# Kernel tuning notes

Hardware: AMD Instinct MI355X
Metric: run time of the kernel (lower is better)

## Reference

```python
import jax, jax.numpy as jnp
import numpy as np

OWN_DIM = 7
INTR_DIM = 5
N_HEADS = 3
HEAD_DIM = 5
N_INTR = 256
ACT_DIM = 2
HID = 256
B = 16384


def setup_inputs() -> dict:
    key = jax.random.key(0)
    ks = jax.random.split(key, 16)
    def rn(k, shape, scale=0.1):
        return (jax.random.normal(k, shape, dtype=jnp.float32) * scale)
    obs = jax.random.normal(ks[0], (B, OWN_DIM + N_INTR * INTR_DIM), dtype=jnp.float32)
    in_dim = OWN_DIM + N_HEADS * HEAD_DIM  # 22
    return {
        "obs": obs,
        "Wq": rn(ks[1], (N_HEADS, HEAD_DIM, OWN_DIM)),
        "bq": rn(ks[2], (N_HEADS, HEAD_DIM)),
        "Wk": rn(ks[3], (N_HEADS, HEAD_DIM, INTR_DIM)),
        "bk": rn(ks[4], (N_HEADS, HEAD_DIM)),
        "Wv": rn(ks[5], (N_HEADS, HEAD_DIM, INTR_DIM)),
        "bv": rn(ks[6], (N_HEADS, HEAD_DIM)),
        "v_att": rn(ks[7], (N_HEADS, HEAD_DIM), 0.5),
        "temperature": jnp.ones((1,), dtype=jnp.float32) * 3.0,
        "W1": rn(ks[8], (in_dim, HID)),
        "b1": rn(ks[9], (HID,)),
        "W2": rn(ks[10], (HID, HID)),
        "b2": rn(ks[11], (HID,)),
        "Wf": rn(ks[12], (HID, ACT_DIM)),
        "bf": rn(ks[13], (ACT_DIM,)),
        "log_std": jnp.zeros((ACT_DIM,), dtype=jnp.float32),
    }


def reference(obs, Wq, bq, Wk, bk, Wv, bv, v_att, temperature,
              W1, b1, W2, b2, Wf, bf, log_std):
    own = obs[:, :OWN_DIM]                                   # [B,7]
    intr = obs[:, OWN_DIM:OWN_DIM + N_INTR * INTR_DIM].reshape(-1, N_INTR, INTR_DIM)  # [B,N,5]

    # per-head projections, all heads at once
    q = jnp.einsum('bo,hdo->bhd', own, Wq) + bq[None]        # [B,H,5]
    k = jnp.einsum('bni,hdi->bhnd', intr, Wk) + bk[None, :, None, :]  # [B,H,N,5]
    v = jnp.einsum('bni,hdi->bhnd', intr, Wv) + bv[None, :, None, :]  # [B,H,N,5]

    energy = jnp.tanh(q[:, :, None, :] + k)                  # [B,H,N,5]
    scores = jnp.einsum('bhnd,hd->bhn', energy, v_att)       # [B,H,N]
    scores = scores * jnp.abs(temperature)[0]

    is_padding = jnp.sum(jnp.abs(intr), axis=2) < 1e-6       # [B,N]
    scores = jnp.where(is_padding[:, None, :], -jnp.inf, scores)
    alpha = jax.nn.softmax(scores, axis=-1)                  # [B,H,N]
    alpha = jnp.nan_to_num(alpha, nan=0.0)

    context = jnp.einsum('bhn,bhnd->bhd', alpha, v).reshape(-1, N_HEADS * HEAD_DIM)  # [B,15]

    x = jnp.concatenate([own, context], axis=1)              # [B,22]
    x = jax.nn.leaky_relu(x @ W1 + b1, negative_slope=0.2)
    x = jax.nn.leaky_relu(x @ W2 + b2, negative_slope=0.2)
    out = x @ Wf + bf                                        # [B,2]
    log_std_exp = jnp.broadcast_to(log_std[None, :], (out.shape[0], ACT_DIM))
    return jnp.concatenate([out, log_std_exp], axis=1)       # [B,4]
```

## Files before the change

### kernel.cpp

```cpp
#include <hip/hip_runtime.h>
#include <math.h>

#define OWN_DIM 7
#define INTR_DIM 5
#define N_HEADS 3
#define HEAD_DIM 5
#define N_INTR 256
#define HID 256
#define BATCH 16384
#define ROW 1287

typedef __attribute__((ext_vector_type(8))) short bf16x8;
typedef __attribute__((ext_vector_type(4))) float f32x4;

__device__ __forceinline__ float fast_tanh(float x) {
    float e = __expf(2.0f * x);
    return 1.0f - 2.0f * __builtin_amdgcn_rcpf(e + 1.0f);
}

__device__ __forceinline__ float leaky(float x) {
    return x > 0.0f ? x : 0.2f * x;
}

__device__ __forceinline__ unsigned short f2bf(float f) {
    union { float f; unsigned u; } v; v.f = f;
    unsigned r = (v.u + 0x7FFFu + ((v.u >> 16) & 1u)) >> 16;
    return (unsigned short)r;
}

__device__ __forceinline__ float bf2f(unsigned short s) {
    union { unsigned u; float f; } v; v.u = ((unsigned)s) << 16;
    return v.f;
}

__global__ __launch_bounds__(256) void attn_w1_kernel(
    const float* __restrict__ obs,
    const float* __restrict__ Wq, const float* __restrict__ bq,
    const float* __restrict__ Wk, const float* __restrict__ bk,
    const float* __restrict__ Wv, const float* __restrict__ bv,
    const float* __restrict__ v_att, const float* __restrict__ temperature,
    const float* __restrict__ W1, const float* __restrict__ b1,
    unsigned short* __restrict__ h1b)
{
    __shared__ float w1s[22 * 256];
    int tid = threadIdx.x;
    for (int i = tid; i < 22 * 256; i += 256) w1s[i] = W1[i];
    __syncthreads();

    int wave = tid >> 6;
    int lane = tid & 63;
    int b = blockIdx.x * 4 + wave;
    const float* row = obs + (size_t)b * ROW;

    float absT = fabsf(temperature[0]);

    float own[7];
    #pragma unroll
    for (int o = 0; o < 7; o++) own[o] = row[o];

    float q[15];
    #pragma unroll
    for (int hd = 0; hd < 15; hd++) {
        float acc = bq[hd];
        #pragma unroll
        for (int o = 0; o < 7; o++) acc = fmaf(own[o], Wq[hd * 7 + o], acc);
        q[hd] = acc;
    }

    float it[4][5];
    float sc[3][4];
    #pragma unroll
    for (int j = 0; j < 4; j++) {
        int n = lane + 64 * j;
        const float* ip = row + OWN_DIM + INTR_DIM * n;
        float asum = 0.0f;
        #pragma unroll
        for (int i = 0; i < 5; i++) { it[j][i] = ip[i]; asum += fabsf(it[j][i]); }
        bool pad = asum < 1e-6f;
        #pragma unroll
        for (int h = 0; h < 3; h++) {
            float s = 0.0f;
            #pragma unroll
            for (int d = 0; d < 5; d++) {
                float kd = bk[h * 5 + d];
                #pragma unroll
                for (int i = 0; i < 5; i++)
                    kd = fmaf(it[j][i], Wk[(h * 5 + d) * 5 + i], kd);
                float e = fast_tanh(q[h * 5 + d] + kd);
                s = fmaf(v_att[h * 5 + d], e, s);
            }
            sc[h][j] = pad ? -INFINITY : s * absT;
        }
    }

    float alpha[3][4];
    float sa[3];
    #pragma unroll
    for (int h = 0; h < 3; h++) {
        float m = fmaxf(fmaxf(sc[h][0], sc[h][1]), fmaxf(sc[h][2], sc[h][3]));
        #pragma unroll
        for (int off = 32; off >= 1; off >>= 1) m = fmaxf(m, __shfl_xor(m, off));
        if (m < -3.0e38f) m = 0.0f;
        float lsum = 0.0f;
        #pragma unroll
        for (int j = 0; j < 4; j++) { alpha[h][j] = __expf(sc[h][j] - m); lsum += alpha[h][j]; }
        #pragma unroll
        for (int off = 32; off >= 1; off >>= 1) lsum += __shfl_xor(lsum, off);
        float rden = lsum > 0.0f ? __builtin_amdgcn_rcpf(lsum) : 0.0f;
        sa[h] = lsum > 0.0f ? 1.0f : 0.0f;
        #pragma unroll
        for (int j = 0; j < 4; j++) alpha[h][j] *= rden;
    }

    float ctx[15];
    #pragma unroll
    for (int hi = 0; hi < 15; hi++) ctx[hi] = 0.0f;
    #pragma unroll
    for (int h = 0; h < 3; h++)
        #pragma unroll
        for (int j = 0; j < 4; j++) {
            float a = alpha[h][j];
            #pragma unroll
            for (int i = 0; i < 5; i++)
                ctx[h * 5 + i] = fmaf(a, it[j][i], ctx[h * 5 + i]);
        }
    #pragma unroll
    for (int hi = 0; hi < 15; hi++) {
        float v = ctx[hi];
        #pragma unroll
        for (int off = 32; off >= 1; off >>= 1) v += __shfl_xor(v, off);
        ctx[hi] = v;
    }

    float x[22];
    #pragma unroll
    for (int o = 0; o < 7; o++) x[o] = own[o];
    #pragma unroll
    for (int hd = 0; hd < 15; hd++) {
        int h = hd / 5;
        float acc = bv[hd] * sa[h];
        #pragma unroll
        for (int i = 0; i < 5; i++)
            acc = fmaf(Wv[hd * 5 + i], ctx[h * 5 + i], acc);
        x[7 + hd] = acc;
    }

    const float4* b1v = (const float4*)b1;
    float4 bb = b1v[lane];
    float accs[4] = { bb.x, bb.y, bb.z, bb.w };
    #pragma unroll
    for (int i = 0; i < 22; i++) {
        const float4 w = *((const float4*)(w1s + i * 256 + 4 * lane));
        accs[0] = fmaf(x[i], w.x, accs[0]);
        accs[1] = fmaf(x[i], w.y, accs[1]);
        accs[2] = fmaf(x[i], w.z, accs[2]);
        accs[3] = fmaf(x[i], w.w, accs[3]);
    }
    ushort4 outv;
    outv.x = f2bf(leaky(accs[0]));
    outv.y = f2bf(leaky(accs[1]));
    outv.z = f2bf(leaky(accs[2]));
    outv.w = f2bf(leaky(accs[3]));
    *((ushort4*)(h1b + (size_t)b * 256 + 4 * lane)) = outv;
}

__global__ __launch_bounds__(256) void mlp_mfma_kernel(
    const unsigned short* __restrict__ h1b, const float* __restrict__ W2,
    const float* __restrict__ b2, unsigned short* __restrict__ h2b)
{
    int tid = threadIdx.x;
    int wave = tid >> 6;
    int lane = tid & 63;
    int lm = lane & 15;
    int q  = lane >> 4;

    int n0 = blockIdx.x * 64 + wave * 16;
    int m_base = blockIdx.y * 128;

    bf16x8 bfrag[8];
    #pragma unroll
    for (int s = 0; s < 8; s++) {
        #pragma unroll
        for (int j = 0; j < 8; j++) {
            int k = s * 32 + q * 8 + j;
            bfrag[s][j] = (short)f2bf(W2[k * 256 + n0 + lm]);
        }
    }

    float bias = b2[n0 + lm];

    #pragma unroll
    for (int mt = 0; mt < 8; mt++) {
        int m0 = m_base + mt * 16;
        const unsigned short* arow = h1b + (size_t)(m0 + lm) * 256 + q * 8;

        f32x4 acc = {0.0f, 0.0f, 0.0f, 0.0f};
        #pragma unroll
        for (int s = 0; s < 8; s++) {
            bf16x8 afrag = *((const bf16x8*)(arow + s * 32));
            acc = __builtin_amdgcn_mfma_f32_16x16x32_bf16(afrag, bfrag[s], acc, 0, 0, 0);
        }
        #pragma unroll
        for (int i = 0; i < 4; i++) {
            int r = m0 + q * 4 + i;
            h2b[(size_t)r * 256 + n0 + lm] = f2bf(leaky(acc[i] + bias));
        }
    }
}

__global__ __launch_bounds__(256) void final_kernel(
    const unsigned short* __restrict__ h2b, const float* __restrict__ Wf,
    const float* __restrict__ bf, const float* __restrict__ log_std,
    float* __restrict__ out)
{
    __shared__ float wfs[512];
    int tid = threadIdx.x;
    for (int i = tid; i < 512; i += 256) wfs[i] = Wf[i];
    __syncthreads();

    int b = blockIdx.x * 256 + tid;
    const uint4* hv = (const uint4*)(h2b + (size_t)b * 256);

    float a0 = 0.0f, a1 = 0.0f;
    #pragma unroll 4
    for (int jj = 0; jj < 32; jj++) {
        uint4 u = hv[jj];
        unsigned w[4] = { u.x, u.y, u.z, u.w };
        #pragma unroll
        for (int p = 0; p < 4; p++) {
            float lo = bf2f((unsigned short)(w[p] & 0xFFFFu));
            float hi = bf2f((unsigned short)(w[p] >> 16));
            int j = jj * 8 + p * 2;
            a0 = fmaf(lo, wfs[(j + 0) * 2 + 0], a0);
            a1 = fmaf(lo, wfs[(j + 0) * 2 + 1], a1);
            a0 = fmaf(hi, wfs[(j + 1) * 2 + 0], a0);
            a1 = fmaf(hi, wfs[(j + 1) * 2 + 1], a1);
        }
    }
    float4 o;
    o.x = a0 + bf[0];
    o.y = a1 + bf[1];
    o.z = log_std[0];
    o.w = log_std[1];
    *((float4*)(out + (size_t)b * 4)) = o;
}

extern "C" void kernel_launch(void* const* d_in, const int* in_sizes, int n_in,
                              void* d_out, int out_size, void* d_ws, size_t ws_size,
                              hipStream_t stream) {
    const float* obs  = (const float*)d_in[0];
    const float* Wq   = (const float*)d_in[1];
    const float* bq   = (const float*)d_in[2];
    const float* Wk   = (const float*)d_in[3];
    const float* bk   = (const float*)d_in[4];
    const float* Wv   = (const float*)d_in[5];
    const float* bv   = (const float*)d_in[6];
    const float* v_att = (const float*)d_in[7];
    const float* temperature = (const float*)d_in[8];
    const float* W1   = (const float*)d_in[9];
    const float* b1   = (const float*)d_in[10];
    const float* W2   = (const float*)d_in[11];
    const float* b2   = (const float*)d_in[12];
    const float* Wf   = (const float*)d_in[13];
    const float* bf   = (const float*)d_in[14];
    const float* log_std = (const float*)d_in[15];
    float* out = (float*)d_out;

    unsigned short* h1b = (unsigned short*)d_ws;
    unsigned short* h2b = h1b + (size_t)BATCH * 256;

    attn_w1_kernel<<<BATCH / 4, 256, 0, stream>>>(
        obs, Wq, bq, Wk, bk, Wv, bv, v_att, temperature, W1, b1, h1b);
    mlp_mfma_kernel<<<dim3(4, 128), 256, 0, stream>>>(h1b, W2, b2, h2b);
    final_kernel<<<BATCH / 256, 256, 0, stream>>>(h2b, Wf, bf, log_std, out);
}
```

Baseline: 196.2 us.

## Fuse W1, W2 and final layers into one MFMA kernel with bf16 weight prep

The attention kernel now writes only a padded 32-wide bf16 input vector per row instead of the 256-wide h1. A new fused kernel computes layer 1 with MFMA, stages h1 through shared memory, runs layer 2 with MFMA, and reduces the final 2-output projection in registers and shared memory. This removes the h1/h2 global round trips and two launches. A small prep kernel pre-transposes and converts W1/W2 to bf16. In exchange, every block loads the whole W2 into registers (high register pressure), each block handles only 32 rows, and layer 1 now runs with bf16 inputs, which costs some precision.

```diff
diff --git a/kernel.cpp b/kernel.cpp
--- a/kernel.cpp
+++ b/kernel.cpp
@@ -28,25 +28,43 @@
     return (unsigned short)r;
 }
 
-__device__ __forceinline__ float bf2f(unsigned short s) {
-    union { unsigned u; float f; } v; v.u = ((unsigned)s) << 16;
-    return v.f;
-}
-
-__global__ __launch_bounds__(256) void attn_w1_kernel(
+__device__ __forceinline__ unsigned pack2(unsigned short a, unsigned short b) {
+    return (unsigned)a | ((unsigned)b << 16);
+}
+
+__global__ __launch_bounds__(256) void prep_kernel(
+    const float* __restrict__ W1, const float* __restrict__ W2,
+    unsigned short* __restrict__ W1t, unsigned short* __restrict__ W2t)
+{
+    int idx = blockIdx.x * 256 + threadIdx.x;
+    int col = idx & 255;
+    int kq = idx >> 8;
+    ushort4 o;
+    o.x = f2bf(W2[(kq * 4 + 0) * 256 + col]);
+    o.y = f2bf(W2[(kq * 4 + 1) * 256 + col]);
+    o.z = f2bf(W2[(kq * 4 + 2) * 256 + col]);
+    o.w = f2bf(W2[(kq * 4 + 3) * 256 + col]);
+    *((ushort4*)(W2t + col * 256 + kq * 4)) = o;
+    if (kq < 8) {
+        ushort4 p;
+        int k = kq * 4;
+        p.x = (k + 0) < 22 ? f2bf(W1[(k + 0) * 256 + col]) : 0;
+        p.y = (k + 1) < 22 ? f2bf(W1[(k + 1) * 256 + col]) : 0;
+        p.z = (k + 2) < 22 ? f2bf(W1[(k + 2) * 256 + col]) : 0;
+        p.w = (k + 3) < 22 ? f2bf(W1[(k + 3) * 256 + col]) : 0;
+        *((ushort4*)(W1t + col * 32 + k)) = p;
+    }
+}
+
+__global__ __launch_bounds__(256) void attn_kernel(
     const float* __restrict__ obs,
     const float* __restrict__ Wq, const float* __restrict__ bq,
     const float* __restrict__ Wk, const float* __restrict__ bk,
     const float* __restrict__ Wv, const float* __restrict__ bv,
     const float* __restrict__ v_att, const float* __restrict__ temperature,
-    const float* __restrict__ W1, const float* __restrict__ b1,
-    unsigned short* __restrict__ h1b)
+    unsigned short* __restrict__ xb)
 {
-    __shared__ float w1s[22 * 256];
     int tid = threadIdx.x;
-    for (int i = tid; i < 22 * 256; i += 256) w1s[i] = W1[i];
-    __syncthreads();
-
     int wave = tid >> 6;
     int lane = tid & 63;
     int b = blockIdx.x * 4 + wave;
@@ -73,9 +91,13 @@
     for (int j = 0; j < 4; j++) {
         int n = lane + 64 * j;
         const float* ip = row + OWN_DIM + INTR_DIM * n;
+        float4 v4;
+        __builtin_memcpy(&v4, ip, 16);
+        it[j][0] = v4.x; it[j][1] = v4.y; it[j][2] = v4.z; it[j][3] = v4.w;
+        it[j][4] = ip[4];
         float asum = 0.0f;
         #pragma unroll
-        for (int i = 0; i < 5; i++) { it[j][i] = ip[i]; asum += fabsf(it[j][i]); }
+        for (int i = 0; i < 5; i++) asum += fabsf(it[j][i]);
         bool pad = asum < 1e-6f;
         #pragma unroll
         for (int h = 0; h < 3; h++) {
@@ -145,104 +167,117 @@
         x[7 + hd] = acc;
     }
 
-    const float4* b1v = (const float4*)b1;
-    float4 bb = b1v[lane];
-    float accs[4] = { bb.x, bb.y, bb.z, bb.w };
-    #pragma unroll
-    for (int i = 0; i < 22; i++) {
-        const float4 w = *((const float4*)(w1s + i * 256 + 4 * lane));
-        accs[0] = fmaf(x[i], w.x, accs[0]);
-        accs[1] = fmaf(x[i], w.y, accs[1]);
-        accs[2] = fmaf(x[i], w.z, accs[2]);
-        accs[3] = fmaf(x[i], w.w, accs[3]);
-    }
-    ushort4 outv;
-    outv.x = f2bf(leaky(accs[0]));
-    outv.y = f2bf(leaky(accs[1]));
-    outv.z = f2bf(leaky(accs[2]));
-    outv.w = f2bf(leaky(accs[3]));
-    *((ushort4*)(h1b + (size_t)b * 256 + 4 * lane)) = outv;
-}
-
-__global__ __launch_bounds__(256) void mlp_mfma_kernel(
-    const unsigned short* __restrict__ h1b, const float* __restrict__ W2,
-    const float* __restrict__ b2, unsigned short* __restrict__ h2b)
+    unsigned short xs[24];
+    #pragma unroll
+    for (int i = 0; i < 22; i++) xs[i] = f2bf(x[i]);
+    xs[22] = 0; xs[23] = 0;
+    uint4 u0 = { pack2(xs[0], xs[1]),  pack2(xs[2], xs[3]),  pack2(xs[4], xs[5]),  pack2(xs[6], xs[7]) };
+    uint4 u1 = { pack2(xs[8], xs[9]),  pack2(xs[10], xs[11]), pack2(xs[12], xs[13]), pack2(xs[14], xs[15]) };
+    uint4 u2 = { pack2(xs[16], xs[17]), pack2(xs[18], xs[19]), pack2(xs[20], xs[21]), pack2(xs[22], xs[23]) };
+    uint4 u3 = { 0u, 0u, 0u, 0u };
+    uint4 lo = (lane & 1) ? u1 : u0;
+    uint4 hi = (lane & 1) ? u3 : u2;
+    uint4 sel = (lane & 2) ? hi : lo;
+    if (lane < 4) {
+        *((uint4*)(xb + (size_t)b * 32 + lane * 8)) = sel;
+    }
+}
+
+__global__ __launch_bounds__(256, 2) void mlp_fused_kernel(
+    const unsigned short* __restrict__ xb,
+    const unsigned short* __restrict__ W1t, const unsigned short* __restrict__ W2t,
+    const float* __restrict__ b1, const float* __restrict__ b2,
+    const float* __restrict__ Wf, const float* __restrict__ bfv,
+    const float* __restrict__ log_std, float* __restrict__ out)
 {
+    __shared__ unsigned short h1t[16 * 264];
+    __shared__ float finbuf[2][4][16][2];
+
     int tid = threadIdx.x;
-    int wave = tid >> 6;
+    int w = tid >> 6;
     int lane = tid & 63;
     int lm = lane & 15;
-    int q  = lane >> 4;
-
-    int n0 = blockIdx.x * 64 + wave * 16;
-    int m_base = blockIdx.y * 128;
-
-    bf16x8 bfrag[8];
-    #pragma unroll
-    for (int s = 0; s < 8; s++) {
-        #pragma unroll
-        for (int j = 0; j < 8; j++) {
-            int k = s * 32 + q * 8 + j;
-            bfrag[s][j] = (short)f2bf(W2[k * 256 + n0 + lm]);
-        }
-    }
-
-    float bias = b2[n0 + lm];
-
-    #pragma unroll
-    for (int mt = 0; mt < 8; mt++) {
-        int m0 = m_base + mt * 16;
-        const unsigned short* arow = h1b + (size_t)(m0 + lm) * 256 + q * 8;
-
-        f32x4 acc = {0.0f, 0.0f, 0.0f, 0.0f};
-        #pragma unroll
-        for (int s = 0; s < 8; s++) {
-            bf16x8 afrag = *((const bf16x8*)(arow + s * 32));
-            acc = __builtin_amdgcn_mfma_f32_16x16x32_bf16(afrag, bfrag[s], acc, 0, 0, 0);
-        }
-        #pragma unroll
-        for (int i = 0; i < 4; i++) {
-            int r = m0 + q * 4 + i;
-            h2b[(size_t)r * 256 + n0 + lm] = f2bf(leaky(acc[i] + bias));
-        }
-    }
-}
-
-__global__ __launch_bounds__(256) void final_kernel(
-    const unsigned short* __restrict__ h2b, const float* __restrict__ Wf,
-    const float* __restrict__ bf, const float* __restrict__ log_std,
-    float* __restrict__ out)
-{
-    __shared__ float wfs[512];
-    int tid = threadIdx.x;
-    for (int i = tid; i < 512; i += 256) wfs[i] = Wf[i];
-    __syncthreads();
-
-    int b = blockIdx.x * 256 + tid;
-    const uint4* hv = (const uint4*)(h2b + (size_t)b * 256);
-
-    float a0 = 0.0f, a1 = 0.0f;
-    #pragma unroll 4
-    for (int jj = 0; jj < 32; jj++) {
-        uint4 u = hv[jj];
-        unsigned w[4] = { u.x, u.y, u.z, u.w };
-        #pragma unroll
-        for (int p = 0; p < 4; p++) {
-            float lo = bf2f((unsigned short)(w[p] & 0xFFFFu));
-            float hi = bf2f((unsigned short)(w[p] >> 16));
-            int j = jj * 8 + p * 2;
-            a0 = fmaf(lo, wfs[(j + 0) * 2 + 0], a0);
-            a1 = fmaf(lo, wfs[(j + 0) * 2 + 1], a1);
-            a0 = fmaf(hi, wfs[(j + 1) * 2 + 0], a0);
-            a1 = fmaf(hi, wfs[(j + 1) * 2 + 1], a1);
-        }
-    }
-    float4 o;
-    o.x = a0 + bf[0];
-    o.y = a1 + bf[1];
-    o.z = log_std[0];
-    o.w = log_std[1];
-    *((float4*)(out + (size_t)b * 4)) = o;
+    int q = lane >> 4;
+    int mbase = blockIdx.x * 32;
+
+    float b1v[4], b2v[4], wf0[4], wf1[4];
+    bf16x8 fw1[4];
+    bf16x8 fw2[4][8];
+    #pragma unroll
+    for (int s = 0; s < 4; s++) {
+        int col = w * 64 + s * 16 + lm;
+        b1v[s] = b1[col];
+        b2v[s] = b2[col];
+        wf0[s] = Wf[col * 2];
+        wf1[s] = Wf[col * 2 + 1];
+        fw1[s] = *((const bf16x8*)(W1t + col * 32 + q * 8));
+        #pragma unroll
+        for (int t = 0; t < 8; t++)
+            fw2[s][t] = *((const bf16x8*)(W2t + col * 256 + t * 32 + q * 8));
+    }
+
+    #pragma unroll
+    for (int mt = 0; mt < 2; mt++) {
+        int m0 = mbase + mt * 16;
+        bf16x8 ax = *((const bf16x8*)(xb + (size_t)(m0 + lm) * 32 + q * 8));
+
+        #pragma unroll
+        for (int s = 0; s < 4; s++) {
+            f32x4 c = {0.0f, 0.0f, 0.0f, 0.0f};
+            c = __builtin_amdgcn_mfma_f32_16x16x32_bf16(ax, fw1[s], c, 0, 0, 0);
+            int col = w * 64 + s * 16 + lm;
+            #pragma unroll
+            for (int i = 0; i < 4; i++)
+                h1t[(q * 4 + i) * 264 + col] = f2bf(leaky(c[i] + b1v[s]));
+        }
+        __syncthreads();
+
+        bf16x8 a2[8];
+        #pragma unroll
+        for (int t = 0; t < 8; t++)
+            a2[t] = *((const bf16x8*)(h1t + lm * 264 + t * 32 + q * 8));
+
+        float p0[4] = {0, 0, 0, 0};
+        float p1[4] = {0, 0, 0, 0};
+        #pragma unroll
+        for (int s = 0; s < 4; s++) {
+            f32x4 acc = {0.0f, 0.0f, 0.0f, 0.0f};
+            #pragma unroll
+            for (int t = 0; t < 8; t++)
+                acc = __builtin_amdgcn_mfma_f32_16x16x32_bf16(a2[t], fw2[s][t], acc, 0, 0, 0);
+            #pragma unroll
+            for (int i = 0; i < 4; i++) {
+                float h2 = leaky(acc[i] + b2v[s]);
+                p0[i] = fmaf(h2, wf0[s], p0[i]);
+                p1[i] = fmaf(h2, wf1[s], p1[i]);
+            }
+        }
+
+        #pragma unroll
+        for (int off = 1; off < 16; off <<= 1) {
+            #pragma unroll
+            for (int i = 0; i < 4; i++) {
+                p0[i] += __shfl_xor(p0[i], off);
+                p1[i] += __shfl_xor(p1[i], off);
+            }
+        }
+        if (lm == 0) {
+            #pragma unroll
+            for (int i = 0; i < 4; i++) {
+                finbuf[mt][w][q * 4 + i][0] = p0[i];
+                finbuf[mt][w][q * 4 + i][1] = p1[i];
+            }
+        }
+        __syncthreads();
+        if (tid < 32) {
+            int r = tid >> 1;
+            int a = tid & 1;
+            float s4 = finbuf[mt][0][r][a] + finbuf[mt][1][r][a]
+                     + finbuf[mt][2][r][a] + finbuf[mt][3][r][a];
+            out[(size_t)(m0 + r) * 4 + a] = s4 + bfv[a];
+            out[(size_t)(m0 + r) * 4 + 2 + a] = log_std[a];
+        }
+    }
 }
 
 extern "C" void kernel_launch(void* const* d_in, const int* in_sizes, int n_in,
@@ -266,11 +301,13 @@
     const float* log_std = (const float*)d_in[15];
     float* out = (float*)d_out;
 
-    unsigned short* h1b = (unsigned short*)d_ws;
-    unsigned short* h2b = h1b + (size_t)BATCH * 256;
-
-    attn_w1_kernel<<<BATCH / 4, 256, 0, stream>>>(
-        obs, Wq, bq, Wk, bk, Wv, bv, v_att, temperature, W1, b1, h1b);
-    mlp_mfma_kernel<<<dim3(4, 128), 256, 0, stream>>>(h1b, W2, b2, h2b);
-    final_kernel<<<BATCH / 256, 256, 0, stream>>>(h2b, Wf, bf, log_std, out);
-}
+    unsigned short* xb  = (unsigned short*)d_ws;
+    unsigned short* W1t = xb + (size_t)BATCH * 32;
+    unsigned short* W2t = W1t + 256 * 32;
+
+    prep_kernel<<<64, 256, 0, stream>>>(W1, W2, W1t, W2t);
+    attn_kernel<<<BATCH / 4, 256, 0, stream>>>(
+        obs, Wq, bq, Wk, bk, Wv, bv, v_att, temperature, xb);
+    mlp_fused_kernel<<<BATCH / 32, 256, 0, stream>>>(
+        xb, W1t, W2t, b1, b2, Wf, bf, log_std, out);
+}
```

New measurement: 185.5 us. -5.4%, faster.
